# Optimization experiments

Measured on AMD Instinct MI355X. Metric: run time of the kernel, lower is better.

## Reference

```python
import jax, jax.numpy as jnp
import numpy as np

B, N, C = 8, 4096, 768
H = 12
D = C // H            # 64
BN = C // 2           # bottleneck dim 384
EPS_LN = 1e-5
EPS_ATTN = 1e-6


def layer_norm(x, g, b):
    mu = jnp.mean(x, axis=-1, keepdims=True)
    var = jnp.mean(jnp.square(x - mu), axis=-1, keepdims=True)
    return (x - mu) * jax.lax.rsqrt(var + EPS_LN) * g + b


def setup_inputs() -> dict:
    key = jax.random.key(0)
    ks = jax.random.split(key, 8)
    s = 0.02
    return {
        "x": jax.random.normal(ks[0], (B, N, C), jnp.float32),
        "w_qkv": jax.random.normal(ks[1], (C, 3 * C), jnp.float32) * s,
        "b_qkv": jnp.zeros((3 * C,), jnp.float32),
        "w_proj": jax.random.normal(ks[2], (C, C), jnp.float32) * s,
        "b_proj": jnp.zeros((C,), jnp.float32),
        "g1": jnp.ones((C,), jnp.float32),
        "beta1": jnp.zeros((C,), jnp.float32),
        "g2": jnp.ones((C,), jnp.float32),
        "beta2": jnp.zeros((C,), jnp.float32),
        "w_down": jax.random.normal(ks[3], (C, BN), jnp.float32) * s,
        "b_down": jnp.zeros((BN,), jnp.float32),
        "w_up": jax.random.normal(ks[4], (BN, C), jnp.float32) * s,
        "b_up": jnp.zeros((C,), jnp.float32),
        "g3": jnp.ones((C,), jnp.float32),
        "beta3": jnp.zeros((C,), jnp.float32),
    }


def _linear_attention(x, w_qkv, b_qkv, w_proj, b_proj):
    # x: (B, N, C)
    qkv = x @ w_qkv + b_qkv                       # (B, N, 3C)
    qkv = qkv.reshape(B, N, 3, H, D)
    qkv = jnp.transpose(qkv, (2, 0, 3, 1, 4))     # (3, B, H, N, D)
    q, k, v = qkv[0], qkv[1], qkv[2]
    fm = lambda t: jax.nn.elu(t) + 1.0            # positive feature map
    q, k = fm(q), fm(k)
    kv = jnp.einsum('bhnd,bhnv->bhdv', k, v)      # (B, H, D, D)
    out = jnp.einsum('bhnd,bhdv->bhnv', q, kv)    # (B, H, N, D)
    k_sum = k.sum(axis=2)                         # (B, H, D)
    normalizer = jnp.einsum('bhnd,bhd->bhn', q, k_sum) + EPS_ATTN
    out = out / normalizer[..., None]
    out = jnp.transpose(out, (0, 2, 1, 3)).reshape(B, N, C)
    return out @ w_proj + b_proj


def reference(x, w_qkv, b_qkv, w_proj, b_proj, g1, beta1, g2, beta2,
              w_down, b_down, w_up, b_up, g3, beta3):
    # DinomalyBlock forward (eval mode: dropout/noise disabled)
    x = x + _linear_attention(layer_norm(x, g1, beta1), w_qkv, b_qkv, w_proj, b_proj)
    r = layer_norm(x, g2, beta2)
    h = jax.nn.gelu(r @ w_down + b_down, approximate=False)  # torch GELU default = exact
    h = h @ w_up + b_up
    return layer_norm(r + h, g3, beta3)
```

## Files before the change

### kernel.cpp

```cpp
#include <hip/hip_runtime.h>
#include <hip/hip_bf16.h>
#include <cstdio>


typedef __attribute__((ext_vector_type(8))) short short8;
typedef __attribute__((ext_vector_type(4))) float floatx4;

__device__ __forceinline__ float bf2f(unsigned short u) {
    return __uint_as_float(((unsigned int)u) << 16);
}
__device__ __forceinline__ unsigned short f2bf(float f) {
    __hip_bfloat16 h = __float2bfloat16(f);
    return *reinterpret_cast<unsigned short*>(&h);
}

__device__ __forceinline__ void async_copy16(const unsigned short* g, unsigned short* l) {
    __builtin_amdgcn_global_load_lds(
        (const __attribute__((address_space(1))) unsigned int*)g,
        (__attribute__((address_space(3))) unsigned int*)l, 16, 0, 0);
}

__device__ __forceinline__ floatx4 MFMA16(short8 a, short8 b, floatx4 c) {
    return __builtin_amdgcn_mfma_f32_16x16x32_bf16(a, b, c, 0, 0, 0);
}

__global__ __launch_bounds__(256) void transpose_all(
    const float* __restrict__ wq, const float* __restrict__ wp,
    const float* __restrict__ wd, const float* __restrict__ wu,
    unsigned short* __restrict__ tq, unsigned short* __restrict__ tp,
    unsigned short* __restrict__ td, unsigned short* __restrict__ tu)
{
    int blk = blockIdx.x;
    const float* w; unsigned short* o; int K, Nc, tx32;
    if (blk < 1728)      { w = wq; o = tq; K = 768; Nc = 2304; tx32 = 24; }
    else if (blk < 2304) { w = wp; o = tp; K = 768; Nc = 768;  tx32 = 24; blk -= 1728; }
    else if (blk < 2592) { w = wd; o = td; K = 768; Nc = 384;  tx32 = 24; blk -= 2304; }
    else                 { w = wu; o = tu; K = 384; Nc = 768;  tx32 = 12; blk -= 2592; }
    int kb = (blk % tx32) * 32, nb = (blk / tx32) * 32;
    __shared__ float tile[32][33];
    int tx = threadIdx.x & 31, ty = threadIdx.x >> 5;
    #pragma unroll
    for (int i = 0; i < 32; i += 8)
        tile[ty + i][tx] = w[(size_t)(kb + ty + i) * Nc + nb + tx];
    __syncthreads();
    #pragma unroll
    for (int i = 0; i < 32; i += 8)
        o[(size_t)(nb + ty + i) * K + kb + tx] = f2bf(tile[tx][ty + i]);
}

template<bool OBF16>
__global__ __launch_bounds__(384) void ln_kernel(
    const float* __restrict__ in, const float* __restrict__ gw,
    const float* __restrict__ bw, void* __restrict__ outp)
{
    int row = blockIdx.x;
    int t = threadIdx.x;
    float2 xv = ((const float2*)(in + (size_t)row * 768))[t];
    float s = xv.x + xv.y;
    float ss = xv.x * xv.x + xv.y * xv.y;
    #pragma unroll
    for (int o = 32; o > 0; o >>= 1) {
        s += __shfl_down(s, o);
        ss += __shfl_down(ss, o);
    }
    __shared__ float red[14];
    int wave = t >> 6, lane = t & 63;
    if (lane == 0) { red[wave] = s; red[6 + wave] = ss; }
    __syncthreads();
    if (t == 0) {
        float S = 0.f, SS = 0.f;
        #pragma unroll
        for (int i = 0; i < 6; i++) { S += red[i]; SS += red[6 + i]; }
        float mu = S * (1.0f / 768.0f);
        float var = SS * (1.0f / 768.0f) - mu * mu;
        red[12] = mu;
        red[13] = rsqrtf(var + 1e-5f);
    }
    __syncthreads();
    float mu = red[12], rstd = red[13];
    float2 g = ((const float2*)gw)[t];
    float2 b = ((const float2*)bw)[t];
    float y0 = (xv.x - mu) * rstd * g.x + b.x;
    float y1 = (xv.y - mu) * rstd * g.y + b.y;
    if (OBF16) {
        unsigned int pk = (unsigned int)f2bf(y0) | ((unsigned int)f2bf(y1) << 16);
        ((unsigned int*)outp)[(size_t)row * 384 + t] = pk;
    } else {
        ((float2*)outp)[(size_t)row * 384 + t] = make_float2(y0, y1);
    }
}

template<bool RES_F32, bool OUT_F32>
__global__ __launch_bounds__(384) void add_ln_kernel(
    const unsigned short* __restrict__ y, const void* __restrict__ resv,
    const float* __restrict__ gw, const float* __restrict__ bw,
    void* __restrict__ outp)
{
    int row = blockIdx.x;
    int t = threadIdx.x;
    unsigned int yp = ((const unsigned int*)(y + (size_t)row * 768))[t];
    float a0 = bf2f((unsigned short)(yp & 0xffff));
    float a1 = bf2f((unsigned short)(yp >> 16));
    float r0, r1;
    if (RES_F32) {
        float2 rv = ((const float2*)((const float*)resv + (size_t)row * 768))[t];
        r0 = rv.x; r1 = rv.y;
    } else {
        unsigned int rp = ((const unsigned int*)((const unsigned short*)resv + (size_t)row * 768))[t];
        r0 = bf2f((unsigned short)(rp & 0xffff));
        r1 = bf2f((unsigned short)(rp >> 16));
    }
    float v0 = a0 + r0, v1 = a1 + r1;
    float s = v0 + v1;
    float ss = v0 * v0 + v1 * v1;
    #pragma unroll
    for (int o = 32; o > 0; o >>= 1) {
        s += __shfl_down(s, o);
        ss += __shfl_down(ss, o);
    }
    __shared__ float red[14];
    int wave = t >> 6, lane = t & 63;
    if (lane == 0) { red[wave] = s; red[6 + wave] = ss; }
    __syncthreads();
    if (t == 0) {
        float S = 0.f, SS = 0.f;
        #pragma unroll
        for (int i = 0; i < 6; i++) { S += red[i]; SS += red[6 + i]; }
        float mu = S * (1.0f / 768.0f);
        float var = SS * (1.0f / 768.0f) - mu * mu;
        red[12] = mu;
        red[13] = rsqrtf(var + 1e-5f);
    }
    __syncthreads();
    float mu = red[12], rstd = red[13];
    float2 g = ((const float2*)gw)[t];
    float2 b = ((const float2*)bw)[t];
    float y0 = (v0 - mu) * rstd * g.x + b.x;
    float y1 = (v1 - mu) * rstd * g.y + b.y;
    if (OUT_F32) {
        ((float2*)outp)[(size_t)row * 384 + t] = make_float2(y0, y1);
    } else {
        unsigned int pk = (unsigned int)f2bf(y0) | ((unsigned int)f2bf(y1) << 16);
        ((unsigned int*)outp)[(size_t)row * 384 + t] = pk;
    }
}

template<int MODE>
__global__ __launch_bounds__(256, 4) void gemm_kernel(
    const unsigned short* __restrict__ A,
    const unsigned short* __restrict__ Wt,
    const float* __restrict__ bias,
    unsigned short* __restrict__ outp,
    int M, int K, int Nc)
{
    __shared__ __align__(16) unsigned short As[128][64];
    __shared__ __align__(16) unsigned short Bs[128][64];
    const int row0 = blockIdx.y * 128;
    const int col0 = blockIdx.x * 128;
    const int t = threadIdx.x;
    const int lane = t & 63;
    const int wave = t >> 6;
    const int wm = (wave >> 1) * 64;
    const int wn = (wave & 1) * 64;
    const int frow = lane & 15;
    const int quad = lane >> 4;
    const int lrow = lane >> 3;
    const int lchunk = (lane & 7) ^ lrow;

    floatx4 acc[4][4];
    #pragma unroll
    for (int i = 0; i < 4; i++)
        #pragma unroll
        for (int j = 0; j < 4; j++)
            acc[i][j] = (floatx4){0.f, 0.f, 0.f, 0.f};

    for (int k0 = 0; k0 < K; k0 += 64) {
        __syncthreads();
        #pragma unroll
        for (int q = 0; q < 4; q++) {
            int r = wave * 32 + q * 8 + lrow;
            async_copy16(A  + (size_t)(row0 + r) * K + k0 + lchunk * 8, &As[wave * 32 + q * 8][0]);
            async_copy16(Wt + (size_t)(col0 + r) * K + k0 + lchunk * 8, &Bs[wave * 32 + q * 8][0]);
        }
        __syncthreads();
        #pragma unroll
        for (int ks = 0; ks < 2; ks++) {
            const int pc = ((ks * 4 + quad) ^ (frow & 7)) * 8;
            short8 af[4], bf4[4];
            #pragma unroll
            for (int i = 0; i < 4; i++) af[i] = *(const short8*)&As[wm + i * 16 + frow][pc];
            #pragma unroll
            for (int j = 0; j < 4; j++) bf4[j] = *(const short8*)&Bs[wn + j * 16 + frow][pc];
            #pragma unroll
            for (int i = 0; i < 4; i++)
                #pragma unroll
                for (int j = 0; j < 4; j++)
                    acc[i][j] = MFMA16(af[i], bf4[j], acc[i][j]);
        }
    }

    #pragma unroll
    for (int i = 0; i < 4; i++) {
        #pragma unroll
        for (int j = 0; j < 4; j++) {
            int col = col0 + wn + j * 16 + frow;
            float bcol = bias[col];
            #pragma unroll
            for (int rr = 0; rr < 4; rr++) {
                int row = row0 + wm + i * 16 + quad * 4 + rr;
                float v = acc[i][j][rr] + bcol;
                if (MODE == 0) {
                    if (col < 1536) v = (v > 0.f) ? (v + 1.f) : expf(v);
                } else if (MODE == 2) {
                    v = 0.5f * v * (1.0f + erff(v * 0.70710678118654752f));
                }
                outp[(size_t)row * Nc + col] = f2bf(v);
            }
        }
    }
}

template<int MODE>
__global__ __launch_bounds__(512, 2) void gemm256(
    const unsigned short* __restrict__ A,
    const unsigned short* __restrict__ Wt,
    const float* __restrict__ bias,
    unsigned short* __restrict__ outp,
    int M, int K, int Nc)
{
    __shared__ __align__(16) unsigned short As[2][2][256][32];
    __shared__ __align__(16) unsigned short Bs[2][2][256][32];

    const int gx = gridDim.x;
    const int nwg = gx * gridDim.y;
    const int lid = blockIdx.y * gx + blockIdx.x;
    const int cpx = nwg >> 3;
    const int swz = (lid & 7) * cpx + (lid >> 3);
    const int row0 = (swz / gx) * 256;
    const int col0 = (swz % gx) * 256;

    const int t = threadIdx.x;
    const int lane = t & 63;
    const int wave = t >> 6;
    const int wm = wave >> 2;
    const int wn = wave & 3;
    const int frow = lane & 15;
    const int quad = lane >> 4;

    const int srow = t >> 2;
    const int gch = ((t & 3) ^ (srow & 3)) * 8;
    const unsigned short* Ag = A  + (size_t)(row0 + srow) * K + gch;
    const unsigned short* Bg = Wt + (size_t)(col0 + srow) * K + gch;
    const size_t rstep = (size_t)128 * K;

    const int nt = K >> 6;

    floatx4 acc[8][4];
    #pragma unroll
    for (int i = 0; i < 8; i++)
        #pragma unroll
        for (int j = 0; j < 4; j++)
            acc[i][j] = (floatx4){0.f, 0.f, 0.f, 0.f};
    short8 af[4], bf[4];

    auto stageA = [&](int slot, int ks, int tile) {
        const unsigned short* g = Ag + (size_t)tile * 64 + ks * 32;
        async_copy16(g,         &As[slot][ks][16 * wave][0]);
        async_copy16(g + rstep, &As[slot][ks][128 + 16 * wave][0]);
    };
    auto stageB = [&](int slot, int ks, int tile) {
        const unsigned short* g = Bg + (size_t)tile * 64 + ks * 32;
        async_copy16(g,         &Bs[slot][ks][16 * wave][0]);
        async_copy16(g + rstep, &Bs[slot][ks][128 + 16 * wave][0]);
    };
    const int pq = (quad ^ (frow & 3)) * 8;
    auto ldA = [&](int slot, int ks, int ch) {
        #pragma unroll
        for (int ii = 0; ii < 4; ii++)
            af[ii] = *(const short8*)&As[slot][ks][wm * 128 + (ch * 4 + ii) * 16 + frow][pq];
    };
    auto ldB = [&](int slot, int ks) {
        #pragma unroll
        for (int j = 0; j < 4; j++)
            bf[j] = *(const short8*)&Bs[slot][ks][wn * 64 + j * 16 + frow][pq];
    };
    auto mm = [&](int ch) {
        __builtin_amdgcn_s_setprio(1);
        #pragma unroll
        for (int ii = 0; ii < 4; ii++)
            #pragma unroll
            for (int j = 0; j < 4; j++)
                acc[ch * 4 + ii][j] = MFMA16(af[ii], bf[j], acc[ch * 4 + ii][j]);
        __builtin_amdgcn_s_setprio(0);
    };

    stageA(0, 0, 0); stageB(0, 0, 0);
    stageA(0, 1, 0); stageB(0, 1, 0);
    stageA(1, 0, 1); stageB(1, 0, 1);
    asm volatile("s_waitcnt vmcnt(4)" ::: "memory");
    __builtin_amdgcn_s_barrier();

    for (int u = 0; u < nt; u++) {
        const int sl = u & 1;
        ldB(sl, 0); ldA(sl, 0, 0);
        if (u + 1 < nt) stageA(sl ^ 1, 1, u + 1);
        __builtin_amdgcn_s_barrier();
        asm volatile("s_waitcnt lgkmcnt(0)" ::: "memory");
        mm(0);
        __builtin_amdgcn_s_barrier();
        ldA(sl, 0, 1);
        if (u + 1 < nt) stageB(sl ^ 1, 1, u + 1);
        __builtin_amdgcn_s_barrier();
        asm volatile("s_waitcnt lgkmcnt(0)" ::: "memory");
        mm(1);
        if (u + 1 < nt) asm volatile("s_waitcnt vmcnt(8)" ::: "memory");
        else            asm volatile("s_waitcnt vmcnt(0)" ::: "memory");
        __builtin_amdgcn_s_barrier();
        ldB(sl, 1); ldA(sl, 1, 0);
        if (u + 2 < nt) stageA(sl, 0, u + 2);
        __builtin_amdgcn_s_barrier();
        asm volatile("s_waitcnt lgkmcnt(0)" ::: "memory");
        mm(0);
        __builtin_amdgcn_s_barrier();
        ldA(sl, 1, 1);
        if (u + 2 < nt) stageB(sl, 0, u + 2);
        __builtin_amdgcn_s_barrier();
        asm volatile("s_waitcnt lgkmcnt(0)" ::: "memory");
        mm(1);
        if (u + 2 < nt) asm volatile("s_waitcnt vmcnt(8)" ::: "memory");
        else            asm volatile("s_waitcnt vmcnt(0)" ::: "memory");
        __builtin_amdgcn_s_barrier();
    }

    #pragma unroll
    for (int i = 0; i < 8; i++) {
        #pragma unroll
        for (int j = 0; j < 4; j++) {
            int col = col0 + wn * 64 + j * 16 + frow;
            float bcol = bias[col];
            #pragma unroll
            for (int rr = 0; rr < 4; rr++) {
                int row = row0 + wm * 128 + i * 16 + quad * 4 + rr;
                float v = acc[i][j][rr] + bcol;
                if (MODE == 0) {
                    if (col < 1536) v = (v > 0.f) ? (v + 1.f) : expf(v);
                } else if (MODE == 2) {
                    v = 0.5f * v * (1.0f + erff(v * 0.70710678118654752f));
                }
                outp[(size_t)row * Nc + col] = f2bf(v);
            }
        }
    }
}

__global__ __launch_bounds__(256) void kv_accum(
    const unsigned short* __restrict__ qkv, float* __restrict__ kvbuf)
{
    int blk = blockIdx.x;
    int chunk = blk & 7;
    int bh = blk >> 3;
    int b = bh / 12, h = bh % 12;
    int n0 = chunk * 512;
    int t = threadIdx.x;
    int d = t & 63, g = t >> 6;
    __shared__ float kl[2][32][68];
    __shared__ float vl[2][32][68];
    float kv[16];
    #pragma unroll
    for (int j = 0; j < 16; j++) kv[j] = 0.f;
    float ks = 0.f;

    int sr = t >> 3;
    int c16 = (t & 7) * 16;
    bool isk = c16 < 64;
    int cc = isk ? c16 : c16 - 64;
    const unsigned short* gbase =
        qkv + (size_t)(b * 4096 + n0 + sr) * 2304 + (isk ? 768 : 1536) + h * 64 + cc;
    uint4 r0, r1;
    auto loadg = [&](int nb) {
        const uint4* s = (const uint4*)(gbase + (size_t)nb * 2304);
        r0 = s[0]; r1 = s[1];
    };
    auto storel = [&](int buf) {
        float* dst = isk ? &kl[buf][sr][cc] : &vl[buf][sr][cc];
        const unsigned short* u0 = (const unsigned short*)&r0;
        const unsigned short* u1 = (const unsigned short*)&r1;
        #pragma unroll
        for (int i = 0; i < 8; i++) dst[i] = bf2f(u0[i]);
        #pragma unroll
        for (int i = 0; i < 8; i++) dst[8 + i] = bf2f(u1[i]);
    };

    loadg(0);
    storel(0);
    __syncthreads();
    for (int c = 0; c < 16; c++) {
        if (c < 15) loadg((c + 1) * 32);
        int bsel = c & 1;
        #pragma unroll 8
        for (int r2 = 0; r2 < 32; r2++) {
            float kd = kl[bsel][r2][d];
            ks += kd;
            const float4* vv = (const float4*)&vl[bsel][r2][g * 16];
            float4 a0 = vv[0], a1 = vv[1], a2 = vv[2], a3 = vv[3];
            kv[0]  += kd * a0.x; kv[1]  += kd * a0.y; kv[2]  += kd * a0.z; kv[3]  += kd * a0.w;
            kv[4]  += kd * a1.x; kv[5]  += kd * a1.y; kv[6]  += kd * a1.z; kv[7]  += kd * a1.w;
            kv[8]  += kd * a2.x; kv[9]  += kd * a2.y; kv[10] += kd * a2.z; kv[11] += kd * a2.w;
            kv[12] += kd * a3.x; kv[13] += kd * a3.y; kv[14] += kd * a3.z; kv[15] += kd * a3.w;
        }
        if (c < 15) storel((c + 1) & 1);
        __syncthreads();
    }
    float* dstg = kvbuf + (size_t)bh * 4160;
    #pragma unroll
    for (int j = 0; j < 16; j++)
        atomicAdd(&dstg[(g * 16 + j) * 64 + d], kv[j]);
    if (g == 0) atomicAdd(&dstg[4096 + d], ks);
}

__global__ __launch_bounds__(256) void attn_apply(
    const unsigned short* __restrict__ qkv, const float* __restrict__ kvbuf,
    unsigned short* __restrict__ attnC)
{
    int blk = blockIdx.x;
    int nchunk = blk & 31;
    int bh = blk >> 5;
    int b = bh / 12, h = bh % 12;
    int n0 = nchunk * 128;
    int t = threadIdx.x;
    int lane = t & 63, wave = t >> 6;
    __shared__ __align__(16) unsigned short ql[128][72];
    __shared__ __align__(16) unsigned short Bs[80][72];

    {
        const float* kvg = kvbuf + (size_t)bh * 4160;
        int e = t >> 2, d0 = (t & 3) * 16;
        const float4* src4 = (const float4*)(kvg + e * 64 + d0);
        #pragma unroll
        for (int i = 0; i < 4; i++) {
            float4 v = src4[i];
            unsigned long long pk = (unsigned long long)f2bf(v.x)
                | ((unsigned long long)f2bf(v.y) << 16)
                | ((unsigned long long)f2bf(v.z) << 32)
                | ((unsigned long long)f2bf(v.w) << 48);
            *(unsigned long long*)&Bs[e][d0 + i * 4] = pk;
        }
        if (t < 64) {
            Bs[64][t] = f2bf(kvg[4096 + t]);
            #pragma unroll
            for (int r = 65; r < 80; r++) Bs[r][t] = 0;
        }
    }
    {
        int r = t >> 1, c0 = (t & 1) * 32;
        const uint4* src = (const uint4*)(qkv + (size_t)(b * 4096 + n0 + r) * 2304 + h * 64 + c0);
        uint4* dst = (uint4*)&ql[r][c0];
        #pragma unroll
        for (int i = 0; i < 4; i++) dst[i] = src[i];
    }
    __syncthreads();

    int frow = lane & 15, quad = lane >> 4;
    floatx4 acc[2][5];
    #pragma unroll
    for (int it = 0; it < 2; it++)
        #pragma unroll
        for (int jt = 0; jt < 5; jt++)
            acc[it][jt] = (floatx4){0.f, 0.f, 0.f, 0.f};

    #pragma unroll
    for (int ks = 0; ks < 2; ks++) {
        int fk = ks * 32 + quad * 8;
        short8 a0 = *(const short8*)&ql[wave * 32 + frow][fk];
        short8 a1 = *(const short8*)&ql[wave * 32 + 16 + frow][fk];
        #pragma unroll
        for (int jt = 0; jt < 5; jt++) {
            short8 bb = *(const short8*)&Bs[jt * 16 + frow][fk];
            acc[0][jt] = __builtin_amdgcn_mfma_f32_16x16x32_bf16(a0, bb, acc[0][jt], 0, 0, 0);
            acc[1][jt] = __builtin_amdgcn_mfma_f32_16x16x32_bf16(a1, bb, acc[1][jt], 0, 0, 0);
        }
    }

    #pragma unroll
    for (int it = 0; it < 2; it++) {
        #pragma unroll
        for (int rr = 0; rr < 4; rr++) {
            float nv = __shfl(acc[it][4][rr], (lane & 48));
            float inv = 1.0f / (nv + 1e-6f);
            int row = n0 + wave * 32 + it * 16 + quad * 4 + rr;
            size_t obase = (size_t)(b * 4096 + row) * 768 + h * 64;
            #pragma unroll
            for (int jt = 0; jt < 4; jt++)
                attnC[obase + jt * 16 + frow] = f2bf(acc[it][jt][rr] * inv);
        }
    }
}

extern "C" void kernel_launch(void* const* d_in, const int* in_sizes, int n_in,
                              void* d_out, int out_size, void* d_ws, size_t ws_size,
                              hipStream_t stream)
{
    const float* x      = (const float*)d_in[0];
    const float* w_qkv  = (const float*)d_in[1];
    const float* b_qkv  = (const float*)d_in[2];
    const float* w_proj = (const float*)d_in[3];
    const float* b_proj = (const float*)d_in[4];
    const float* g1     = (const float*)d_in[5];
    const float* be1    = (const float*)d_in[6];
    const float* g2     = (const float*)d_in[7];
    const float* be2    = (const float*)d_in[8];
    const float* w_down = (const float*)d_in[9];
    const float* b_down = (const float*)d_in[10];
    const float* w_up   = (const float*)d_in[11];
    const float* b_up   = (const float*)d_in[12];
    const float* g3     = (const float*)d_in[13];
    const float* be3    = (const float*)d_in[14];

    char* p = (char*)d_ws;
    auto take = [&](size_t b) { char* q = p; p += (b + 255) & ~(size_t)255; return q; };
    unsigned short* wtq  = (unsigned short*)take((size_t)2304 * 768 * 2);
    unsigned short* wtp  = (unsigned short*)take((size_t)768 * 768 * 2);
    unsigned short* wtd  = (unsigned short*)take((size_t)384 * 768 * 2);
    unsigned short* wtu  = (unsigned short*)take((size_t)768 * 384 * 2);
    unsigned short* bufA = (unsigned short*)take((size_t)32768 * 768 * 2);
    unsigned short* qkvb = (unsigned short*)take((size_t)32768 * 2304 * 2);
    float*          kvb  = (float*)take((size_t)96 * 4160 * 4);
    unsigned short* hbuf = (unsigned short*)take((size_t)32768 * 384 * 2);
    unsigned short* rbuf    = qkvb;
    unsigned short* projout = qkvb + (size_t)32768 * 768;
    unsigned short* upout   = qkvb + (size_t)2 * 32768 * 768;

    size_t needed = (size_t)(p - (char*)d_ws);
    if (needed > ws_size)
        fprintf(stderr, "WARNING: ws too small: need %zu have %zu\n", needed, ws_size);

    transpose_all<<<2880, 256, 0, stream>>>(w_qkv, w_proj, w_down, w_up, wtq, wtp, wtd, wtu);
    hipMemsetAsync(kvb, 0, (size_t)96 * 4160 * 4, stream);

    ln_kernel<true><<<32768, 384, 0, stream>>>(x, g1, be1, bufA);
    gemm256<0><<<dim3(9, 128), 512, 0, stream>>>(bufA, wtq, b_qkv, qkvb, 32768, 768, 2304);
    kv_accum<<<768, 256, 0, stream>>>(qkvb, kvb);
    attn_apply<<<3072, 256, 0, stream>>>(qkvb, kvb, bufA);
    gemm256<1><<<dim3(3, 128), 512, 0, stream>>>(bufA, wtp, b_proj, projout, 32768, 768, 768);
    add_ln_kernel<true, false><<<32768, 384, 0, stream>>>(projout, x, g2, be2, rbuf);
    gemm_kernel<2><<<dim3(3, 256), 256, 0, stream>>>(rbuf, wtd, b_down, hbuf, 32768, 768, 384);
    gemm256<1><<<dim3(3, 128), 512, 0, stream>>>(hbuf, wtu, b_up, upout, 32768, 384, 768);
    add_ln_kernel<false, true><<<32768, 384, 0, stream>>>(upout, rbuf, g3, be3, (float*)d_out);
}
```

Baseline: 742.1 us.

## Use 64-wide swizzled LDS rows and single-tile-ahead prefetch in gemm256

The A/B shared-memory tiles change from two 32-column k-halves into one 64-column row, with an 8-way XOR swizzle on 16-byte chunks. Each wave now stages 8 full rows, so 8 lanes cover one contiguous 128-byte global row segment, which should give better-coalesced async global-to-LDS copies. The pipeline now prefetches the next K tile in four half-tile pieces instead of staying two half-stages ahead, with `s_waitcnt vmcnt` points adjusted to match. Less prefetch lead time may expose more global-load latency, and the new swizzle changes the LDS bank-conflict pattern.

```diff
diff --git a/kernel.cpp b/kernel.cpp
--- a/kernel.cpp
+++ b/kernel.cpp
@@ -228,8 +228,8 @@
     unsigned short* __restrict__ outp,
     int M, int K, int Nc)
 {
-    __shared__ __align__(16) unsigned short As[2][2][256][32];
-    __shared__ __align__(16) unsigned short Bs[2][2][256][32];
+    __shared__ __align__(16) unsigned short As[2][256][64];
+    __shared__ __align__(16) unsigned short Bs[2][256][64];
 
     const int gx = gridDim.x;
     const int nwg = gx * gridDim.y;
@@ -247,11 +247,10 @@
     const int frow = lane & 15;
     const int quad = lane >> 4;
 
-    const int srow = t >> 2;
-    const int gch = ((t & 3) ^ (srow & 3)) * 8;
-    const unsigned short* Ag = A  + (size_t)(row0 + srow) * K + gch;
-    const unsigned short* Bg = Wt + (size_t)(col0 + srow) * K + gch;
-    const size_t rstep = (size_t)128 * K;
+    const int lrow = lane >> 3;
+    const int lch  = (lane & 7) ^ lrow;
+    const unsigned short* Ag = A  + (size_t)(row0 + wave * 8 + lrow) * K + lch * 8;
+    const unsigned short* Bg = Wt + (size_t)(col0 + wave * 8 + lrow) * K + lch * 8;
 
     const int nt = K >> 6;
 
@@ -263,72 +262,71 @@
             acc[i][j] = (floatx4){0.f, 0.f, 0.f, 0.f};
     short8 af[4], bf[4];
 
-    auto stageA = [&](int slot, int ks, int tile) {
-        const unsigned short* g = Ag + (size_t)tile * 64 + ks * 32;
-        async_copy16(g,         &As[slot][ks][16 * wave][0]);
-        async_copy16(g + rstep, &As[slot][ks][128 + 16 * wave][0]);
-    };
-    auto stageB = [&](int slot, int ks, int tile) {
-        const unsigned short* g = Bg + (size_t)tile * 64 + ks * 32;
-        async_copy16(g,         &Bs[slot][ks][16 * wave][0]);
-        async_copy16(g + rstep, &Bs[slot][ks][128 + 16 * wave][0]);
-    };
-    const int pq = (quad ^ (frow & 3)) * 8;
-    auto ldA = [&](int slot, int ks, int ch) {
+    auto stageA = [&](int slot, int h, int tile) {
+        const unsigned short* g = Ag + (size_t)tile * 64;
+        async_copy16(g + (size_t)(h * 64) * K,        &As[slot][h * 64 + wave * 8][0]);
+        async_copy16(g + (size_t)(128 + h * 64) * K,  &As[slot][128 + h * 64 + wave * 8][0]);
+    };
+    auto stageB = [&](int slot, int h, int tile) {
+        const unsigned short* g = Bg + (size_t)tile * 64;
+        async_copy16(g + (size_t)(h * 64) * K,        &Bs[slot][h * 64 + wave * 8][0]);
+        async_copy16(g + (size_t)(128 + h * 64) * K,  &Bs[slot][128 + h * 64 + wave * 8][0]);
+    };
+    auto ldA = [&](int slot, int ks, int ih) {
+        const int pc = ((ks * 4 + quad) ^ (frow & 7)) * 8;
         #pragma unroll
         for (int ii = 0; ii < 4; ii++)
-            af[ii] = *(const short8*)&As[slot][ks][wm * 128 + (ch * 4 + ii) * 16 + frow][pq];
+            af[ii] = *(const short8*)&As[slot][wm * 128 + ih * 64 + ii * 16 + frow][pc];
     };
     auto ldB = [&](int slot, int ks) {
+        const int pc = ((ks * 4 + quad) ^ (frow & 7)) * 8;
         #pragma unroll
         for (int j = 0; j < 4; j++)
-            bf[j] = *(const short8*)&Bs[slot][ks][wn * 64 + j * 16 + frow][pq];
-    };
-    auto mm = [&](int ch) {
+            bf[j] = *(const short8*)&Bs[slot][wn * 64 + j * 16 + frow][pc];
+    };
+    auto mm = [&](int ih) {
         __builtin_amdgcn_s_setprio(1);
         #pragma unroll
         for (int ii = 0; ii < 4; ii++)
             #pragma unroll
             for (int j = 0; j < 4; j++)
-                acc[ch * 4 + ii][j] = MFMA16(af[ii], bf[j], acc[ch * 4 + ii][j]);
+                acc[ih * 4 + ii][j] = MFMA16(af[ii], bf[j], acc[ih * 4 + ii][j]);
         __builtin_amdgcn_s_setprio(0);
     };
 
-    stageA(0, 0, 0); stageB(0, 0, 0);
-    stageA(0, 1, 0); stageB(0, 1, 0);
-    stageA(1, 0, 1); stageB(1, 0, 1);
-    asm volatile("s_waitcnt vmcnt(4)" ::: "memory");
+    stageB(0, 0, 0); stageB(0, 1, 0);
+    stageA(0, 0, 0); stageA(0, 1, 0);
+    asm volatile("s_waitcnt vmcnt(0)" ::: "memory");
     __builtin_amdgcn_s_barrier();
 
     for (int u = 0; u < nt; u++) {
         const int sl = u & 1;
         ldB(sl, 0); ldA(sl, 0, 0);
-        if (u + 1 < nt) stageA(sl ^ 1, 1, u + 1);
+        if (u + 1 < nt) stageB(sl ^ 1, 0, u + 1);
         __builtin_amdgcn_s_barrier();
         asm volatile("s_waitcnt lgkmcnt(0)" ::: "memory");
         mm(0);
+        if (u + 1 < nt) asm volatile("s_waitcnt vmcnt(2)" ::: "memory");
+        else            asm volatile("s_waitcnt vmcnt(0)" ::: "memory");
         __builtin_amdgcn_s_barrier();
         ldA(sl, 0, 1);
         if (u + 1 < nt) stageB(sl ^ 1, 1, u + 1);
         __builtin_amdgcn_s_barrier();
         asm volatile("s_waitcnt lgkmcnt(0)" ::: "memory");
         mm(1);
-        if (u + 1 < nt) asm volatile("s_waitcnt vmcnt(8)" ::: "memory");
-        else            asm volatile("s_waitcnt vmcnt(0)" ::: "memory");
         __builtin_amdgcn_s_barrier();
         ldB(sl, 1); ldA(sl, 1, 0);
-        if (u + 2 < nt) stageA(sl, 0, u + 2);
+        if (u + 1 < nt) stageA(sl ^ 1, 0, u + 1);
         __builtin_amdgcn_s_barrier();
         asm volatile("s_waitcnt lgkmcnt(0)" ::: "memory");
         mm(0);
         __builtin_amdgcn_s_barrier();
         ldA(sl, 1, 1);
-        if (u + 2 < nt) stageB(sl, 0, u + 2);
+        if (u + 1 < nt) stageA(sl ^ 1, 1, u + 1);
         __builtin_amdgcn_s_barrier();
         asm volatile("s_waitcnt lgkmcnt(0)" ::: "memory");
         mm(1);
-        if (u + 2 < nt) asm volatile("s_waitcnt vmcnt(8)" ::: "memory");
-        else            asm volatile("s_waitcnt vmcnt(0)" ::: "memory");
+        asm volatile("s_waitcnt vmcnt(2)" ::: "memory");
         __builtin_amdgcn_s_barrier();
     }
 
```

Result: faster. 720.0 us (-3.0%).
